# Kernel optimization log

Measured on AMD Instinct MI355X. Metric: run time of the kernel, lower is better.

## Reference

```python
import jax, jax.numpy as jnp
import numpy as np

DIM = 768
HEADS = 12
HEAD_DIM = DIM // HEADS
SCALE = HEAD_DIM ** -0.5
ALPHA = 0.1


def setup_inputs() -> dict:
    key = jax.random.key(0)
    ks = jax.random.split(key, 6)
    B, N, C = 16, 577, DIM
    x = jax.random.normal(ks[0], (B, N, C), dtype=jnp.float32)
    attn_weight = jax.random.uniform(ks[1], (B, N - 1), dtype=jnp.float32)
    w_qkv = jax.random.normal(ks[2], (C, 3 * C), dtype=jnp.float32) * (C ** -0.5)
    b_qkv = jnp.zeros((3 * C,), dtype=jnp.float32)
    w_proj = jax.random.normal(ks[3], (C, C), dtype=jnp.float32) * (C ** -0.5)
    b_proj = jnp.zeros((C,), dtype=jnp.float32)
    return {"x": x, "attn_weight": attn_weight, "w_qkv": w_qkv, "b_qkv": b_qkv,
            "w_proj": w_proj, "b_proj": b_proj}


def reference(x, attn_weight, w_qkv, b_qkv, w_proj, b_proj):
    B, N, C = x.shape
    H, D = HEADS, HEAD_DIM
    qkv = (x @ w_qkv + b_qkv).reshape(B, N, 3, H, D)
    qkv = jnp.transpose(qkv, (2, 0, 3, 1, 4))  # [3, B, H, N, D]
    q, k, v = qkv[0], qkv[1], qkv[2]
    attn = jnp.einsum('bhnd,bhmd->bhnm', q, k) * SCALE  # [B,H,N,N]
    patch_attn = attn[:, :, 0, 1:]  # pre-softmax CLS->patch scores
    # reweight CLS row (excluding CLS->CLS) before softmax
    w = attn_weight[:, None, None, :]  # [B,1,1,N-1]
    cls_row = attn[:, :, 0:1, 1:] * (w * ALPHA + (1.0 - ALPHA))
    attn = attn.at[:, :, 0:1, 1:].set(cls_row)
    attn = jax.nn.softmax(attn, axis=-1)
    out = jnp.einsum('bhnm,bhmd->bhnd', attn, v)
    out = jnp.transpose(out, (0, 2, 1, 3)).reshape(B, N, C)
    out = out @ w_proj + b_proj
    return out, patch_attn
```

## Files before the change

### kernel.cpp

```cpp
#include <hip/hip_runtime.h>
#include <hip/hip_bf16.h>
#include <math.h>

#define B_    16
#define N_    577
#define C_    768
#define H_    12
#define D_    64
#define M_    (B_ * N_)
#define MP_   9344
#define QKVN  2304
#define NP_   640
#define SCALE 0.125f
#define ALPHA 0.1f
#define OUT0  (B_ * N_ * C_)

#define NB_CONV 7008
#define NB_T1   1728
#define NB_T2   576

typedef __attribute__((ext_vector_type(8))) short short8;
typedef __attribute__((ext_vector_type(4))) float f32x4;
typedef __hip_bfloat16 bf16;

__device__ __forceinline__ float exp2fast(float x) {
    return __builtin_amdgcn_exp2f(x);
}

__device__ __forceinline__ void load16(const void* g, void* l) {
    __builtin_amdgcn_global_load_lds(
        (const __attribute__((address_space(1))) unsigned int*)g,
        (__attribute__((address_space(3))) unsigned int*)l, 16, 0, 0);
}

__device__ __forceinline__ f32x4 mfma16(short8 a, short8 b, f32x4 c) {
    return __builtin_amdgcn_mfma_f32_16x16x32_bf16(a, b, c, 0, 0, 0);
}

#define FENCE() asm volatile("" ::: "memory")
#define BARRIER() do { FENCE(); __builtin_amdgcn_s_barrier(); FENCE(); } while (0)
#define WAITLGKM0() asm volatile("s_waitcnt lgkmcnt(0)" ::: "memory")

__global__ __launch_bounds__(256) void prep(const float* __restrict__ x,
                                            bf16* __restrict__ xb,
                                            const float* __restrict__ wq,
                                            bf16* __restrict__ wqT,
                                            const float* __restrict__ wp,
                                            bf16* __restrict__ wpT) {
    __shared__ float tile[32][33];
    const int bid = blockIdx.x;
    if (bid < NB_CONV) {
        int idx = bid * 256 + threadIdx.x;
        int m = idx / 192;
        bf16 tmp[4];
        if (m < M_) {
            float4 f = ((const float4*)x)[idx];
            tmp[0] = __float2bfloat16(f.x);
            tmp[1] = __float2bfloat16(f.y);
            tmp[2] = __float2bfloat16(f.z);
            tmp[3] = __float2bfloat16(f.w);
        } else {
            tmp[0] = tmp[1] = tmp[2] = tmp[3] = __float2bfloat16(0.f);
        }
        ((ushort4*)xb)[idx] = *(ushort4*)tmp;
        return;
    }
    const float* src; bf16* dst; int C, R, bx, by;
    if (bid < NB_CONV + NB_T1) {
        int r = bid - NB_CONV;
        bx = r % 72; by = r / 72; src = wq; dst = wqT; R = 768; C = QKVN;
    } else {
        int r = bid - NB_CONV - NB_T1;
        bx = r % 24; by = r / 24; src = wp; dst = wpT; R = 768; C = 768;
    }
    int cb = bx * 32, rb = by * 32;
    int tx = threadIdx.x & 31, ty = threadIdx.x >> 5;
    #pragma unroll
    for (int i = 0; i < 32; i += 8)
        tile[ty + i][tx] = src[(size_t)(rb + ty + i) * C + cb + tx];
    __syncthreads();
    #pragma unroll
    for (int i = 0; i < 32; i += 8)
        dst[(size_t)(cb + ty + i) * R + rb + tx] = __float2bfloat16(tile[tx][ty + i]);
}

__global__ __launch_bounds__(512, 2) void gemm256(const bf16* __restrict__ A,
                                                  const bf16* __restrict__ BT,
                                                  const float* __restrict__ bias,
                                                  bf16* __restrict__ q,
                                                  bf16* __restrict__ kk,
                                                  bf16* __restrict__ vt,
                                                  float* __restrict__ out,
                                                  int mode, int nby) {
    __shared__ __align__(16) char smem[131072];

    const int nwg = gridDim.x;
    const int orig = blockIdx.x;
    const int xcd = orig & 7, ii = orig >> 3;
    const int qq = nwg >> 3, rr = nwg & 7;
    const int wg = (xcd < rr ? xcd * (qq + 1) : rr * (qq + 1) + (xcd - rr) * qq) + ii;
    const int mb = wg / nby;
    const int nb = wg - mb * nby;
    const int m0 = mb * 256, n0 = nb * 256;
    const int t = threadIdx.x, lane = t & 63, w = t >> 6;
    const int wr = w >> 2, wc = w & 3;
    const int r16 = lane & 15, quad = lane >> 4;

    f32x4 acc[8][4];
    #pragma unroll
    for (int i = 0; i < 8; i++)
        #pragma unroll
        for (int j = 0; j < 4; j++) acc[i][j] = (f32x4)(0.f);

    const int lrow = lane >> 3;
    const int clog = ((lane & 7) ^ lrow) << 4;
    const int s2 = w * 2;
    const char* gA = (const char*)A  + (size_t)(m0 + lrow) * 1536 + clog;
    const char* gB = (const char*)BT + (size_t)(n0 + lrow) * 1536 + clog;

    auto stage = [&](int kt2) {
        const int bo = (kt2 & 1) * 32768;
        const int kc = kt2 * 128;
        #pragma unroll
        for (int half = 0; half < 2; half++) {
            int ro = (half * 128 + s2 * 8) * 1536 + kc;
            char* dA = (char*)smem + bo + half * 16384 + s2 * 1024;
            char* dB = dA + 65536;
            load16(gA + ro, dA);
            load16(gA + ro + 8 * 1536, dA + 1024);
            load16(gB + ro, dB);
            load16(gB + ro + 8 * 1536, dB + 1024);
        }
    };

    stage(0);
    stage(1);
    asm volatile("s_waitcnt vmcnt(8)" ::: "memory");
    BARRIER();

    const int sw = r16 & 7;
    const int g0 = (quad ^ sw) << 4;
    const int g1 = ((quad ^ 4) ^ sw) << 4;

    auto tile = [&](int k, bool doStage, int vmN) {
        const int cur = k & 1;
        const char* Ap = (const char*)smem + cur * 32768 + (wr * 128 + r16) * 128;
        const char* Bp = (const char*)smem + 65536 + cur * 32768 + (wc * 64 + r16) * 128;
        short8 af[4], bf[4];

        #pragma unroll
        for (int mi = 0; mi < 4; mi++) af[mi] = *(const short8*)(Ap + mi * 2048 + g0);
        #pragma unroll
        for (int nj = 0; nj < 4; nj++) bf[nj] = *(const short8*)(Bp + nj * 2048 + g0);
        BARRIER();
        WAITLGKM0();
        __builtin_amdgcn_s_setprio(1);
        #pragma unroll
        for (int mi = 0; mi < 4; mi++)
            #pragma unroll
            for (int nj = 0; nj < 4; nj++)
                acc[mi][nj] = mfma16(af[mi], bf[nj], acc[mi][nj]);
        __builtin_amdgcn_s_setprio(0);
        BARRIER();

        #pragma unroll
        for (int mi = 0; mi < 4; mi++) af[mi] = *(const short8*)(Ap + (mi + 4) * 2048 + g0);
        BARRIER();
        WAITLGKM0();
        __builtin_amdgcn_s_setprio(1);
        #pragma unroll
        for (int mi = 0; mi < 4; mi++)
            #pragma unroll
            for (int nj = 0; nj < 4; nj++)
                acc[mi + 4][nj] = mfma16(af[mi], bf[nj], acc[mi + 4][nj]);
        __builtin_amdgcn_s_setprio(0);
        BARRIER();

        #pragma unroll
        for (int mi = 0; mi < 4; mi++) af[mi] = *(const short8*)(Ap + mi * 2048 + g1);
        #pragma unroll
        for (int nj = 0; nj < 4; nj++) bf[nj] = *(const short8*)(Bp + nj * 2048 + g1);
        BARRIER();
        WAITLGKM0();
        __builtin_amdgcn_s_setprio(1);
        #pragma unroll
        for (int mi = 0; mi < 4; mi++)
            #pragma unroll
            for (int nj = 0; nj < 4; nj++)
                acc[mi][nj] = mfma16(af[mi], bf[nj], acc[mi][nj]);
        __builtin_amdgcn_s_setprio(0);
        BARRIER();

        #pragma unroll
        for (int mi = 0; mi < 4; mi++) af[mi] = *(const short8*)(Ap + (mi + 4) * 2048 + g1);
        BARRIER();
        WAITLGKM0();
        if (doStage) stage(k + 2);
        __builtin_amdgcn_s_setprio(1);
        #pragma unroll
        for (int mi = 0; mi < 4; mi++)
            #pragma unroll
            for (int nj = 0; nj < 4; nj++)
                acc[mi + 4][nj] = mfma16(af[mi], bf[nj], acc[mi + 4][nj]);
        __builtin_amdgcn_s_setprio(0);
        if (vmN == 8)      { asm volatile("s_waitcnt vmcnt(8)" ::: "memory"); }
        else if (vmN == 0) { asm volatile("s_waitcnt vmcnt(0)" ::: "memory"); }
        BARRIER();
    };

    #pragma unroll 1
    for (int kp = 0; kp < 5; kp++) {
        tile(2 * kp,     true, 8);
        tile(2 * kp + 1, true, 8);
    }
    tile(10, false, 0);
    tile(11, false, -1);

    float bs[4];
    #pragma unroll
    for (int nj = 0; nj < 4; nj++) bs[nj] = bias[n0 + wc * 64 + nj * 16 + r16];

    if (mode == 1) {
        #pragma unroll
        for (int mi = 0; mi < 8; mi++) {
            #pragma unroll
            for (int nj = 0; nj < 4; nj++) {
                #pragma unroll
                for (int r = 0; r < 4; r++) {
                    int m = m0 + wr * 128 + mi * 16 + quad * 4 + r;
                    if (m >= M_) continue;
                    out[(size_t)m * 768 + n0 + wc * 64 + nj * 16 + r16] = acc[mi][nj][r] + bs[nj];
                }
            }
        }
        return;
    }

    bf16* Tt = (bf16*)smem;
    const int part = nb / 3;
    const int h0 = (nb % 3) * 4;

    #pragma unroll
    for (int rh = 0; rh < 2; rh++) {
        __syncthreads();
        if (wr == rh) {
            #pragma unroll
            for (int mi = 0; mi < 8; mi++) {
                #pragma unroll
                for (int nj = 0; nj < 4; nj++) {
                    bf16 pk[4];
                    #pragma unroll
                    for (int r = 0; r < 4; r++)
                        pk[r] = __float2bfloat16(acc[mi][nj][r] + bs[nj]);
                    int ccl = wc * 64 + nj * 16 + r16;
                    int ml4 = mi * 16 + quad * 4;
                    *(uint2*)&Tt[ccl * 140 + ml4] = *(const uint2*)pk;
                }
            }
        }
        __syncthreads();
        if (part < 2) {
            int nl = t & 127, hq = t >> 7;
            int m = m0 + rh * 128 + nl;
            if (m < M_) {
                int b = m / N_, n = m - b * N_;
                bf16* dst = (part == 0 ? q : kk) + ((size_t)(b * H_ + h0 + hq) * N_ + n) * 64;
                #pragma unroll
                for (int d8 = 0; d8 < 8; d8++) {
                    bf16 tv[8];
                    #pragma unroll
                    for (int dd = 0; dd < 8; dd++)
                        tv[dd] = Tt[(hq * 64 + d8 * 8 + dd) * 140 + nl];
                    *(uint4*)(dst + d8 * 8) = *(const uint4*)tv;
                }
            }
        } else {
            int dr = t >> 1, seg = t & 1;
            int rem = (nb % 3) * 256 + dr;
            int h = rem >> 6, d = rem & 63;
            int mb2 = m0 + rh * 128 + seg * 64;
            int b = mb2 / N_;
            int n = mb2 - b * N_;
            const bf16* src = Tt + dr * 140 + seg * 64;
            int i = 0;
            while (i < 64 && mb2 + i < M_) {
                if (n == N_) { b++; n = 0; }
                bf16* drow = vt + ((size_t)(b * H_ + h) * 64 + d) * NP_;
                if ((n & 7) == 0 && n + 8 <= N_ && i + 8 <= 64 && mb2 + i + 8 <= M_) {
                    bf16 tv[8];
                    #pragma unroll
                    for (int dd = 0; dd < 8; dd++) tv[dd] = src[i + dd];
                    *(uint4*)(drow + n) = *(const uint4*)tv;
                    i += 8; n += 8;
                } else {
                    drow[n] = src[i]; i++; n++;
                }
            }
        }
    }
}

__global__ __launch_bounds__(256) void attn_mfma(const bf16* __restrict__ q,
                                                 const bf16* __restrict__ k,
                                                 const bf16* __restrict__ vt,
                                                 const float* __restrict__ aw,
                                                 bf16* __restrict__ ao,
                                                 float* __restrict__ patch) {
    __shared__ bf16 Kb[2][4096];
    __shared__ bf16 Vb[2][4096];
    __shared__ bf16 Pb[4][2048];
    const int bh = blockIdx.x, qt = blockIdx.y;
    const int b = bh / H_, h = bh - b * H_;
    const int t = threadIdx.x, lane = t & 63, w = t >> 6;
    const int r16 = lane & 15, quad = lane >> 4;
    const float SC2 = SCALE * 1.44269504f;

    const bf16* kbp = k + (size_t)bh * N_ * 64;
    const bf16* vbp = vt + (size_t)bh * 64 * NP_;

    short8 qa0[2], qa1[2];
    #pragma unroll
    for (int mi = 0; mi < 2; mi++) {
        int qrow = qt * 128 + w * 32 + mi * 16 + r16;
        int qrc = (qrow < N_) ? qrow : (N_ - 1);
        const bf16* qp = q + ((size_t)bh * N_ + qrc) * 64 + quad * 8;
        qa0[mi] = *(const short8*)(qp);
        qa1[mi] = *(const short8*)(qp + 32);
    }

    f32x4 Oacc[2][4];
    #pragma unroll
    for (int mi = 0; mi < 2; mi++)
        #pragma unroll
        for (int d0 = 0; d0 < 4; d0++) Oacc[mi][d0] = (f32x4)(0.f);
    float lrow[2][4];
    #pragma unroll
    for (int mi = 0; mi < 2; mi++)
        #pragma unroll
        for (int rr = 0; rr < 4; rr++) lrow[mi][rr] = 0.f;

    const bool clsrow = (qt == 0) && (w == 0) && (quad == 0);

    auto stage = [&](int kt, int buf) {
        #pragma unroll
        for (int is = 0; is < 2; is++) {
            int base = is * 256 + w * 64;
            int slot = base + lane;
            int row = slot >> 3, pos = slot & 7;
            int c = pos ^ (row & 7);
            int jg = kt * 64 + row; if (jg > N_ - 1) jg = N_ - 1;
            load16(kbp + (size_t)jg * 64 + c * 8, &Kb[buf][base * 8]);
        }
        #pragma unroll
        for (int is = 0; is < 2; is++) {
            int base = is * 256 + w * 64;
            int slot = base + lane;
            int row = slot >> 3, pos = slot & 7;
            int c = pos ^ (row & 7);
            load16(vbp + (size_t)row * NP_ + kt * 64 + c * 8, &Vb[buf][base * 8]);
        }
    };

    stage(0, 0);
    __syncthreads();

    for (int kt = 0; kt < 10; kt++) {
        const int cur = kt & 1;
        if (kt < 9) stage(kt + 1, cur ^ 1);

        f32x4 S[2][4];
        #pragma unroll
        for (int j0 = 0; j0 < 4; j0++) {
            int row = j0 * 16 + r16;
            const bf16* kpl = &Kb[cur][row * 64];
            short8 kf0 = *(const short8*)(kpl + ((quad ^ (row & 7)) << 3));
            short8 kf1 = *(const short8*)(kpl + (((quad ^ 4) ^ (row & 7)) << 3));
            #pragma unroll
            for (int mi = 0; mi < 2; mi++) {
                f32x4 sa = (f32x4)(0.f);
                sa = mfma16(qa0[mi], kf0, sa);
                sa = mfma16(qa1[mi], kf1, sa);
                S[mi][j0] = sa;
            }
        }

        if (kt < 9) {
            #pragma unroll
            for (int mi = 0; mi < 2; mi++) {
                #pragma unroll
                for (int j0 = 0; j0 < 4; j0++) {
                    float wfac = 1.f;
                    if (mi == 0 && clsrow) {
                        int c = kt * 64 + j0 * 16 + r16;
                        if (c >= 1) {
                            patch[(size_t)bh * (N_ - 1) + (c - 1)] = S[0][j0][0] * SCALE;
                            wfac = aw[b * (N_ - 1) + (c - 1)] * ALPHA + (1.f - ALPHA);
                        }
                    }
                    #pragma unroll
                    for (int rr = 0; rr < 4; rr++) {
                        float v = S[mi][j0][rr] * SC2;
                        if (rr == 0) v *= wfac;
                        float p = exp2fast(v);
                        S[mi][j0][rr] = p;
                        lrow[mi][rr] += p;
                    }
                }
            }
        } else {
            #pragma unroll
            for (int mi = 0; mi < 2; mi++) {
                #pragma unroll
                for (int j0 = 0; j0 < 4; j0++) {
                    int c = kt * 64 + j0 * 16 + r16;
                    bool valid = (c < N_);
                    float wfac = 1.f;
                    if (mi == 0 && clsrow && valid) {
                        patch[(size_t)bh * (N_ - 1) + (c - 1)] = S[0][j0][0] * SCALE;
                        wfac = aw[b * (N_ - 1) + (c - 1)] * ALPHA + (1.f - ALPHA);
                    }
                    #pragma unroll
                    for (int rr = 0; rr < 4; rr++) {
                        float v = S[mi][j0][rr] * SC2;
                        if (rr == 0) v *= wfac;
                        float p = valid ? exp2fast(v) : 0.f;
                        S[mi][j0][rr] = p;
                        lrow[mi][rr] += p;
                    }
                }
            }
        }

        bf16* pw = &Pb[w][0];
        #pragma unroll
        for (int mi = 0; mi < 2; mi++) {
            #pragma unroll
            for (int j0 = 0; j0 < 4; j0++) {
                int cg = j0 * 2 + (r16 >> 3);
                #pragma unroll
                for (int rr = 0; rr < 4; rr++) {
                    int rp = mi * 16 + quad * 4 + rr;
                    pw[rp * 64 + ((cg ^ (rp & 7)) << 3) + (r16 & 7)] =
                        __float2bfloat16(S[mi][j0][rr]);
                }
            }
        }
        short8 pa0[2], pa1[2];
        #pragma unroll
        for (int mi = 0; mi < 2; mi++) {
            int rp = mi * 16 + r16;
            const bf16* pr = pw + rp * 64;
            pa0[mi] = *(const short8*)(pr + ((quad ^ (rp & 7)) << 3));
            pa1[mi] = *(const short8*)(pr + (((quad ^ 4) ^ (rp & 7)) << 3));
        }

        #pragma unroll
        for (int d0 = 0; d0 < 4; d0++) {
            int row = d0 * 16 + r16;
            const bf16* vpl = &Vb[cur][row * 64];
            short8 vf0 = *(const short8*)(vpl + ((quad ^ (row & 7)) << 3));
            short8 vf1 = *(const short8*)(vpl + (((quad ^ 4) ^ (row & 7)) << 3));
            #pragma unroll
            for (int mi = 0; mi < 2; mi++) {
                Oacc[mi][d0] = mfma16(pa0[mi], vf0, Oacc[mi][d0]);
                Oacc[mi][d0] = mfma16(pa1[mi], vf1, Oacc[mi][d0]);
            }
        }
        __syncthreads();
    }

    #pragma unroll
    for (int mi = 0; mi < 2; mi++) {
        #pragma unroll
        for (int rr = 0; rr < 4; rr++) {
            float l = lrow[mi][rr];
            l += __shfl_xor(l, 1);
            l += __shfl_xor(l, 2);
            l += __shfl_xor(l, 4);
            l += __shfl_xor(l, 8);
            int n = qt * 128 + w * 32 + mi * 16 + quad * 4 + rr;
            if (n >= N_) continue;
            float inv = 1.f / l;
            #pragma unroll
            for (int d0 = 0; d0 < 4; d0++) {
                ao[((size_t)(b * N_ + n) * H_ + h) * 64 + d0 * 16 + r16] =
                    __float2bfloat16(Oacc[mi][d0][rr] * inv);
            }
        }
    }
}

extern "C" void kernel_launch(void* const* d_in, const int* in_sizes, int n_in,
                              void* d_out, int out_size, void* d_ws, size_t ws_size,
                              hipStream_t stream) {
    const float* x      = (const float*)d_in[0];
    const float* aw     = (const float*)d_in[1];
    const float* w_qkv  = (const float*)d_in[2];
    const float* b_qkv  = (const float*)d_in[3];
    const float* w_proj = (const float*)d_in[4];
    const float* b_proj = (const float*)d_in[5];
    float* out = (float*)d_out;

    char* ws = (char*)d_ws;
    bf16* xbf    = (bf16*)(ws);
    bf16* wqkvT  = (bf16*)(ws + 14352384);
    bf16* wprojT = (bf16*)(ws + 17891328);
    bf16* qv     = (bf16*)(ws + 19070976);
    bf16* kv     = (bf16*)(ws + 33251328);
    bf16* vt     = (bf16*)(ws + 47431680);
    bf16* ao     = xbf;

    prep<<<NB_CONV + NB_T1 + NB_T2, 256, 0, stream>>>(x, xbf, w_qkv, wqkvT, w_proj, wprojT);

    gemm256<<<37 * 9, 512, 0, stream>>>(
        xbf, wqkvT, b_qkv, qv, kv, vt, nullptr, 0, 9);

    attn_mfma<<<dim3(H_ * B_, 5), 256, 0, stream>>>(qv, kv, vt, aw, ao, out + OUT0);

    gemm256<<<37 * 3, 512, 0, stream>>>(
        ao, wprojT, b_proj, nullptr, nullptr, nullptr, out, 1, 3);
}
```

Baseline: 238.8 us.

## Simplify GEMM mainloop to one-ahead prefetch with a single barrier per tile

Restructures the bf16 MFMA GEMM main loop. It now issues the global-to-LDS load for tile k+1 at the start of tile k and waits on vmcnt(0) plus one barrier at the end of each tile. Previously it prefetched two tiles ahead and placed barriers and lgkmcnt waits around every quarter of the MFMA work. The aim is to remove most of the intra-tile barrier and wait overhead. In exchange, prefetch depth drops to one tile and each tile ends with a full wait on outstanding global loads, which may expose more memory latency.

```diff
diff --git a/kernel.cpp b/kernel.cpp
--- a/kernel.cpp
+++ b/kernel.cpp
@@ -39,7 +39,6 @@
 
 #define FENCE() asm volatile("" ::: "memory")
 #define BARRIER() do { FENCE(); __builtin_amdgcn_s_barrier(); FENCE(); } while (0)
-#define WAITLGKM0() asm volatile("s_waitcnt lgkmcnt(0)" ::: "memory")
 
 __global__ __launch_bounds__(256) void prep(const float* __restrict__ x,
                                             bf16* __restrict__ xb,
@@ -134,87 +133,76 @@
     };
 
     stage(0);
-    stage(1);
-    asm volatile("s_waitcnt vmcnt(8)" ::: "memory");
+    asm volatile("s_waitcnt vmcnt(0)" ::: "memory");
     BARRIER();
 
     const int sw = r16 & 7;
     const int g0 = (quad ^ sw) << 4;
     const int g1 = ((quad ^ 4) ^ sw) << 4;
 
-    auto tile = [&](int k, bool doStage, int vmN) {
+    auto tile = [&](int k, bool notlast) {
         const int cur = k & 1;
         const char* Ap = (const char*)smem + cur * 32768 + (wr * 128 + r16) * 128;
         const char* Bp = (const char*)smem + 65536 + cur * 32768 + (wc * 64 + r16) * 128;
-        short8 af[4], bf[4];
-
-        #pragma unroll
-        for (int mi = 0; mi < 4; mi++) af[mi] = *(const short8*)(Ap + mi * 2048 + g0);
-        #pragma unroll
-        for (int nj = 0; nj < 4; nj++) bf[nj] = *(const short8*)(Bp + nj * 2048 + g0);
-        BARRIER();
-        WAITLGKM0();
+        short8 a[4], bfr[4];
+
+        if (notlast) stage(k + 1);
+
+        #pragma unroll
+        for (int mi = 0; mi < 4; mi++) a[mi] = *(const short8*)(Ap + mi * 2048 + g0);
+        #pragma unroll
+        for (int nj = 0; nj < 4; nj++) bfr[nj] = *(const short8*)(Bp + nj * 2048 + g0);
         __builtin_amdgcn_s_setprio(1);
         #pragma unroll
         for (int mi = 0; mi < 4; mi++)
             #pragma unroll
             for (int nj = 0; nj < 4; nj++)
-                acc[mi][nj] = mfma16(af[mi], bf[nj], acc[mi][nj]);
+                acc[mi][nj] = mfma16(a[mi], bfr[nj], acc[mi][nj]);
         __builtin_amdgcn_s_setprio(0);
-        BARRIER();
-
-        #pragma unroll
-        for (int mi = 0; mi < 4; mi++) af[mi] = *(const short8*)(Ap + (mi + 4) * 2048 + g0);
-        BARRIER();
-        WAITLGKM0();
+
+        #pragma unroll
+        for (int mi = 0; mi < 4; mi++) a[mi] = *(const short8*)(Ap + (mi + 4) * 2048 + g0);
         __builtin_amdgcn_s_setprio(1);
         #pragma unroll
         for (int mi = 0; mi < 4; mi++)
             #pragma unroll
             for (int nj = 0; nj < 4; nj++)
-                acc[mi + 4][nj] = mfma16(af[mi], bf[nj], acc[mi + 4][nj]);
+                acc[mi + 4][nj] = mfma16(a[mi], bfr[nj], acc[mi + 4][nj]);
         __builtin_amdgcn_s_setprio(0);
-        BARRIER();
-
-        #pragma unroll
-        for (int mi = 0; mi < 4; mi++) af[mi] = *(const short8*)(Ap + mi * 2048 + g1);
-        #pragma unroll
-        for (int nj = 0; nj < 4; nj++) bf[nj] = *(const short8*)(Bp + nj * 2048 + g1);
-        BARRIER();
-        WAITLGKM0();
+
+        #pragma unroll
+        for (int mi = 0; mi < 4; mi++) a[mi] = *(const short8*)(Ap + mi * 2048 + g1);
+        #pragma unroll
+        for (int nj = 0; nj < 4; nj++) bfr[nj] = *(const short8*)(Bp + nj * 2048 + g1);
         __builtin_amdgcn_s_setprio(1);
         #pragma unroll
         for (int mi = 0; mi < 4; mi++)
             #pragma unroll
             for (int nj = 0; nj < 4; nj++)
-                acc[mi][nj] = mfma16(af[mi], bf[nj], acc[mi][nj]);
+                acc[mi][nj] = mfma16(a[mi], bfr[nj], acc[mi][nj]);
         __builtin_amdgcn_s_setprio(0);
-        BARRIER();
-
-        #pragma unroll
-        for (int mi = 0; mi < 4; mi++) af[mi] = *(const short8*)(Ap + (mi + 4) * 2048 + g1);
-        BARRIER();
-        WAITLGKM0();
-        if (doStage) stage(k + 2);
+
+        #pragma unroll
+        for (int mi = 0; mi < 4; mi++) a[mi] = *(const short8*)(Ap + (mi + 4) * 2048 + g1);
         __builtin_amdgcn_s_setprio(1);
         #pragma unroll
         for (int mi = 0; mi < 4; mi++)
             #pragma unroll
             for (int nj = 0; nj < 4; nj++)
-                acc[mi + 4][nj] = mfma16(af[mi], bf[nj], acc[mi + 4][nj]);
+                acc[mi + 4][nj] = mfma16(a[mi], bfr[nj], acc[mi + 4][nj]);
         __builtin_amdgcn_s_setprio(0);
-        if (vmN == 8)      { asm volatile("s_waitcnt vmcnt(8)" ::: "memory"); }
-        else if (vmN == 0) { asm volatile("s_waitcnt vmcnt(0)" ::: "memory"); }
+
+        if (notlast) { asm volatile("s_waitcnt vmcnt(0)" ::: "memory"); }
         BARRIER();
     };
 
     #pragma unroll 1
     for (int kp = 0; kp < 5; kp++) {
-        tile(2 * kp,     true, 8);
-        tile(2 * kp + 1, true, 8);
-    }
-    tile(10, false, 0);
-    tile(11, false, -1);
+        tile(2 * kp,     true);
+        tile(2 * kp + 1, true);
+    }
+    tile(10, true);
+    tile(11, false);
 
     float bs[4];
     #pragma unroll
```

Result: faster. 231.3 us (-3.1%).
